# Kernel tuning notes

Hardware: AMD Instinct MI355X
Metric: run time of the kernel (lower is better)

Reference implementation:

```python
import jax, jax.numpy as jnp
import numpy as np
from jax import lax

E = 300   # word embedding dim (hard-coded embedding_size in DMCNN)
P = 5     # position-feature dim
H = 200   # conv out channels
S = 256   # max_seq_len
L = 34    # num_labels
VOCAB = 21128


def setup_inputs() -> dict:
    key = jax.random.key(0)
    ks = jax.random.split(key, 7)
    B = 8
    return {
        "inputs": jax.random.randint(ks[0], (B, S), 0, VOCAB, dtype=jnp.int64),
        "word_emb": jax.random.normal(ks[1], (VOCAB, E), dtype=jnp.float32) * 0.02,
        "pf_emb": jax.random.normal(ks[2], (S, P), dtype=jnp.float32) * 0.02,
        "conv_W": jax.random.normal(ks[3], (H, E + P, 3), dtype=jnp.float32) * 0.02,
        "conv_b": jax.random.normal(ks[4], (H,), dtype=jnp.float32) * 0.02,
        "fc_W": jax.random.normal(ks[5], (L, 3 * E + 2 * H), dtype=jnp.float32) * 0.02,
        "fc_b": jax.random.normal(ks[6], (L,), dtype=jnp.float32) * 0.02,
    }


def _conv1d(x_ncs, w_oik):
    # x: [N, C, S], w: [O, I, K], stride 1, padding 1 (kernel 3)
    return lax.conv_general_dilated(
        x_ncs, w_oik, window_strides=(1,), padding=[(1, 1)],
        dimension_numbers=("NCH", "OIH", "NCH"))


def reference(inputs, word_emb, pf_emb, conv_W, conv_b, fc_W, fc_b):
    B = inputs.shape[0]
    tok = word_emb[inputs]                       # [B, S, E]

    # Positions i = 1 .. S-2 (the original loop), fully vectorized.
    i_vals = jnp.arange(1, S - 1)                # [S-2]
    j = jnp.arange(S)
    pos_idx = jnp.abs(j[None, :] - i_vals[:, None])   # [S-2, S] == the loop's pos_index
    pf = pf_emb[pos_idx]                         # [S-2, S, P]

    # Conv is linear: split into token part (shared across i) + pf part (per i).
    W_tok, W_pf = conv_W[:, :E, :], conv_W[:, E:, :]
    conv_tok = _conv1d(tok.transpose(0, 2, 1), W_tok) + conv_b[None, :, None]  # [B, H, S]
    conv_pf = _conv1d(pf.transpose(0, 2, 1), W_pf)                             # [S-2, H, S] (batch-independent)

    out = jax.nn.relu(conv_tok[None] + conv_pf[:, None])   # [S-2, B, H, S]

    # Dynamic split max-pool at index i.
    left_mask = (j[None, :] < i_vals[:, None])[:, None, None, :]  # [S-2,1,1,S]
    neg_inf = jnp.array(-jnp.inf, dtype=out.dtype)
    max_left = jnp.where(left_mask, out, neg_inf).max(axis=-1)    # [S-2, B, H]
    max_right = jnp.where(left_mask, neg_inf, out).max(axis=-1)   # [S-2, B, H]
    pool = jnp.concatenate([max_left, max_right], axis=-1)        # [S-2, B, 2H]

    # Lexical-level features: window [i-1, i, i+1] flattened.
    llf = jnp.concatenate([tok[:, 0:S - 2], tok[:, 1:S - 1], tok[:, 2:S]], axis=-1)  # [B, S-2, 3E]

    feat = jnp.concatenate([pool.transpose(1, 0, 2), llf], axis=-1)  # [B, S-2, 2H+3E]
    logits_mid = jnp.einsum("bsf,lf->bsl", feat, fc_W) + fc_b        # [B, S-2, L]

    pad = jnp.zeros((B, 1, L), dtype=logits_mid.dtype).at[:, :, -1].set(1.0)
    return jnp.concatenate([pad, logits_mid, pad], axis=1)          # [B, S, L]
```

## Files before the change

### kernel.cpp

```cpp
#include <hip/hip_runtime.h>

#define E 300
#define P 5
#define H 200
#define S 256
#define L 34
#define B 8
#define NI 254

typedef __attribute__((ext_vector_type(8))) _Float16 half8;
typedef __attribute__((ext_vector_type(2))) _Float16 h2;
typedef __attribute__((ext_vector_type(4))) float f32x4;

#define TOKB_OFF   0
#define TOKB_FL    309632
#define WR3_OFF    309632
#define WR3_FL     96512
#define FCWB_OFF   406144
#define FCWB_FL    32256
#define G_OFF      438400
#define G_FL       51200
#define C0_OFF     489600
#define C0_FL      25400
#define C255_OFF   515000
#define C255_FL    25400
#define CT_OFF     540400
#define CT_FL      204800
#define POOLF_OFF  745200
#define POOLF_FL   425984

__device__ __forceinline__ unsigned short f2h(float f) {
    _Float16 h = (_Float16)f;
    unsigned short u; __builtin_memcpy(&u, &h, 2);
    return u;
}
__device__ __forceinline__ h2 u2h2(unsigned u) {
    h2 h; __builtin_memcpy(&h, &u, 4); return h;
}
__device__ __forceinline__ unsigned h2u(h2 h) {
    unsigned u; __builtin_memcpy(&u, &h, 4); return u;
}
__device__ __forceinline__ h2 hmax2(h2 a, h2 b) {
    return __builtin_elementwise_max(a, b);
}
__device__ __forceinline__ half8 load_h8(const unsigned short* p) {
    half8 r;
    ((ushort4*)&r)[0] = *(const ushort4*)p;
    ((ushort4*)&r)[1] = *(const ushort4*)(p + 4);
    return r;
}

#define GA_BLOCKS 605
#define PREP_BLOCKS 1803

__global__ __launch_bounds__(256) void k_init(const int* __restrict__ ids,
                                              const float* __restrict__ we,
                                              const float* __restrict__ convW,
                                              const float* __restrict__ fcW,
                                              const float* __restrict__ pf,
                                              unsigned short* __restrict__ tokb,
                                              unsigned short* __restrict__ Wr3,
                                              unsigned short* __restrict__ fcWb,
                                              unsigned short* __restrict__ g,
                                              unsigned short* __restrict__ c0,
                                              unsigned short* __restrict__ c255) {
    if (blockIdx.x < GA_BLOCKS) {
        int idx = blockIdx.x * 256 + threadIdx.x;
        const int total = B * 258 * 75;
        if (idx >= total) return;
        int row = idx / 75;
        int col = idx - row * 75;
        int b = row / 258;
        int r = row - b * 258;
        float4 v = make_float4(0.f, 0.f, 0.f, 0.f);
        if (r >= 1 && r <= 256) {
            int id = ids[b * S + (r - 1)];
            v = ((const float4*)we)[(size_t)id * 75 + col];
        }
        ushort4 o;
        o.x = f2h(v.x); o.y = f2h(v.y); o.z = f2h(v.z); o.w = f2h(v.w);
        *(ushort4*)(tokb + (size_t)row * 300 + col * 4) = o;
        return;
    }
    int idx = (blockIdx.x - GA_BLOCKS) * 256 + threadIdx.x;
    if (idx < 193024) {
        int hh = idx / 928, kk = idx - hh * 928;
        float v = 0.f;
        if (hh < H && kk < 900) {
            int r = kk / 300, e = kk - r * 300;
            v = convW[hh * 915 + e * 3 + r];
        }
        Wr3[idx] = f2h(v);
    } else if (idx < 257536) {
        int t = idx - 193024;
        int l = t / 1344, c = t - l * 1344;
        float v = 0.f;
        if (l < L) {
            if (c < 400) v = fcW[l * 1300 + c];
            else if (c >= 416 && c < 1316) v = fcW[l * 1300 + 400 + (c - 416)];
        }
        fcWb[t] = f2h(v);
    } else if (idx < 359936) {
        int t = idx - 257536;
        int t2 = t / H, h = t - t2 * H;
        int d = t2 - 256;
        float a = 0.f;
#pragma unroll
        for (int k = 0; k < 3; k++) {
            int r = d + k - 1; r = (r < 0) ? -r : r; if (r > 255) r = 255;
#pragma unroll
            for (int q = 0; q < P; q++)
                a += convW[h * 915 + (E + q) * 3 + k] * pf[r * P + q];
        }
        g[t] = f2h(a);
    } else if (idx < 410736) {
        int t = idx - 359936;
        int m = t / H, h = t - m * H;
        int i = m + 1;
        float a = 0.f;
#pragma unroll
        for (int q = 0; q < P; q++) {
            a += convW[h * 915 + (E + q) * 3 + 1] * pf[i * P + q];
            a += convW[h * 915 + (E + q) * 3 + 2] * pf[(i - 1) * P + q];
        }
        c0[m * H + h] = f2h(a);
    } else if (idx < 461536) {
        int t = idx - 410736;
        int m = t / H, h = t - m * H;
        int i = m + 1;
        float a = 0.f;
#pragma unroll
        for (int q = 0; q < P; q++) {
            a += convW[h * 915 + (E + q) * 3 + 0] * pf[(254 - i) * P + q];
            a += convW[h * 915 + (E + q) * 3 + 1] * pf[(255 - i) * P + q];
        }
        c255[m * H + h] = f2h(a);
    }
}

__global__ __launch_bounds__(512) void k_conv(const unsigned short* __restrict__ tokb,
                                              const unsigned short* __restrict__ Wr3,
                                              const float* __restrict__ convB,
                                              unsigned short* __restrict__ ct) {
    __shared__ float4 cld[4 * 64];
    int n0 = blockIdx.x * 16;
    int mg = blockIdx.y;
    int tid = threadIdx.x;
    int wave = tid >> 6;
    int lane = tid & 63;
    int mt = wave & 3;
    int kh = wave >> 2;
    int quad = lane >> 4;
    int lr = lane & 15;
    int mtile = mg * 4 + mt;
    int b = mtile >> 4;
    int j0 = (mtile & 15) << 4;

    const unsigned short* pa = tokb + ((size_t)(b * 258 + j0 + lr) * 300 + quad * 8);
    const unsigned short* pb = Wr3 + ((size_t)(n0 + lr) * 928 + quad * 8);

    f32x4 acc0 = {0.f, 0.f, 0.f, 0.f};
    f32x4 acc1 = {0.f, 0.f, 0.f, 0.f};
    if (kh == 0) {
#pragma unroll
        for (int kk = 0; kk < 14; kk += 2) {
            half8 a0 = load_h8(pa + kk * 32);
            half8 b0 = load_h8(pb + kk * 32);
            acc0 = __builtin_amdgcn_mfma_f32_16x16x32_f16(a0, b0, acc0, 0, 0, 0);
            half8 a1 = load_h8(pa + kk * 32 + 32);
            half8 b1 = load_h8(pb + kk * 32 + 32);
            acc1 = __builtin_amdgcn_mfma_f32_16x16x32_f16(a1, b1, acc1, 0, 0, 0);
        }
    } else {
#pragma unroll
        for (int kk = 14; kk + 1 < 29; kk += 2) {
            half8 a0 = load_h8(pa + kk * 32);
            half8 b0 = load_h8(pb + kk * 32);
            acc0 = __builtin_amdgcn_mfma_f32_16x16x32_f16(a0, b0, acc0, 0, 0, 0);
            half8 a1 = load_h8(pa + kk * 32 + 32);
            half8 b1 = load_h8(pb + kk * 32 + 32);
            acc1 = __builtin_amdgcn_mfma_f32_16x16x32_f16(a1, b1, acc1, 0, 0, 0);
        }
        {
            half8 a0 = load_h8(pa + 28 * 32);
            half8 b0 = load_h8(pb + 28 * 32);
            acc0 = __builtin_amdgcn_mfma_f32_16x16x32_f16(a0, b0, acc0, 0, 0, 0);
        }
    }
    f32x4 accw = acc0 + acc1;
    if (kh == 1) {
        cld[mt * 64 + lane] = make_float4(accw[0], accw[1], accw[2], accw[3]);
    }
    __syncthreads();
    if (kh == 0) {
        float4 p = cld[mt * 64 + lane];
        int h = n0 + lr;
        if (h < H) {
            float bias = convB[h];
            ct[(size_t)(b * 256 + j0 + quad * 4 + 0) * 200 + h] = f2h(accw[0] + p.x + bias);
            ct[(size_t)(b * 256 + j0 + quad * 4 + 1) * 200 + h] = f2h(accw[1] + p.y + bias);
            ct[(size_t)(b * 256 + j0 + quad * 4 + 2) * 200 + h] = f2h(accw[2] + p.z + bias);
            ct[(size_t)(b * 256 + j0 + quad * 4 + 3) * 200 + h] = f2h(accw[3] + p.w + bias);
        }
    }
}

__global__ __launch_bounds__(512) void k_poolA(const unsigned short* __restrict__ ct,
                                               const unsigned short* __restrict__ g,
                                               const unsigned short* __restrict__ c0,
                                               const unsigned short* __restrict__ c255,
                                               unsigned short* __restrict__ poolf) {
    __shared__ uint2 lds2[8 * 4 * 2 * 50];
    int pg = blockIdx.x;
    int b  = blockIdx.y;
    int tid = threadIdx.x;
    int sub = tid >> 6;
    int lane = tid & 63;
    int p0 = pg * 4 + 1;

    if (lane < 50) {
        int h = lane << 2;
        const unsigned short* ctb = ct + (size_t)b * S * H + h;
        const unsigned short* gb  = g + h;

        h2 z = {(_Float16)0, (_Float16)0};
        h2 aL0a=z, aL0b=z, aL1a=z, aL1b=z, aL2a=z, aL2b=z, aL3a=z, aL3b=z;
        h2 aR0a=z, aR0b=z, aR1a=z, aR1b=z, aR2a=z, aR2b=z, aR3a=z, aR3b=z;

        if (sub == 0) {
            uint2 cu = *(const uint2*)ctb;
            h2 ca = u2h2(cu.x), cb = u2h2(cu.y);
            int m = pg * 4;
            if (m + 0 < NI) { uint2 t = *(const uint2*)(c0 + (m+0) * H + h);
                aL0a = hmax2(aL0a, ca + u2h2(t.x)); aL0b = hmax2(aL0b, cb + u2h2(t.y)); }
            if (m + 1 < NI) { uint2 t = *(const uint2*)(c0 + (m+1) * H + h);
                aL1a = hmax2(aL1a, ca + u2h2(t.x)); aL1b = hmax2(aL1b, cb + u2h2(t.y)); }
            if (m + 2 < NI) { uint2 t = *(const uint2*)(c0 + (m+2) * H + h);
                aL2a = hmax2(aL2a, ca + u2h2(t.x)); aL2b = hmax2(aL2b, cb + u2h2(t.y)); }
            if (m + 3 < NI) { uint2 t = *(const uint2*)(c0 + (m+3) * H + h);
                aL3a = hmax2(aL3a, ca + u2h2(t.x)); aL3b = hmax2(aL3b, cb + u2h2(t.y)); }
        }
        if (sub == 7) {
            uint2 cu = *(const uint2*)(ctb + (size_t)255 * H);
            h2 ca = u2h2(cu.x), cb = u2h2(cu.y);
            int m = pg * 4;
            if (m + 0 < NI) { uint2 t = *(const uint2*)(c255 + (m+0) * H + h);
                aR0a = hmax2(aR0a, ca + u2h2(t.x)); aR0b = hmax2(aR0b, cb + u2h2(t.y)); }
            if (m + 1 < NI) { uint2 t = *(const uint2*)(c255 + (m+1) * H + h);
                aR1a = hmax2(aR1a, ca + u2h2(t.x)); aR1b = hmax2(aR1b, cb + u2h2(t.y)); }
            if (m + 2 < NI) { uint2 t = *(const uint2*)(c255 + (m+2) * H + h);
                aR2a = hmax2(aR2a, ca + u2h2(t.x)); aR2b = hmax2(aR2b, cb + u2h2(t.y)); }
            if (m + 3 < NI) { uint2 t = *(const uint2*)(c255 + (m+3) * H + h);
                aR3a = hmax2(aR3a, ca + u2h2(t.x)); aR3b = hmax2(aR3b, cb + u2h2(t.y)); }
        }

        int js = (sub == 0) ? 1 : sub * 32;
        int je = (sub == 7) ? 254 : sub * 32 + 31;

        uint2 gu;
        gu = *(const uint2*)(gb + (size_t)(js - p0 + 256) * H); h2 gr0a = u2h2(gu.x), gr0b = u2h2(gu.y);
        gu = *(const uint2*)(gb + (size_t)(js - p0 + 255) * H); h2 gr1a = u2h2(gu.x), gr1b = u2h2(gu.y);
        gu = *(const uint2*)(gb + (size_t)(js - p0 + 254) * H); h2 gr2a = u2h2(gu.x), gr2b = u2h2(gu.y);
        gu = *(const uint2*)(gb + (size_t)(js - p0 + 253) * H); h2 gr3a = u2h2(gu.x), gr3b = u2h2(gu.y);

        int eL = (je + 1 < p0) ? (je + 1) : p0;
        int mS = (js > p0) ? js : p0;
        int eM = (je + 1 < p0 + 4) ? (je + 1) : (p0 + 4);
        int rS = (js > p0 + 4) ? js : (p0 + 4);

#pragma unroll 4
        for (int j = js; j < eL; ++j) {
            uint2 cu = *(const uint2*)(ctb + (size_t)j * H);
            h2 ca = u2h2(cu.x), cb = u2h2(cu.y);
            aL0a = hmax2(aL0a, ca + gr0a); aL0b = hmax2(aL0b, cb + gr0b);
            aL1a = hmax2(aL1a, ca + gr1a); aL1b = hmax2(aL1b, cb + gr1b);
            aL2a = hmax2(aL2a, ca + gr2a); aL2b = hmax2(aL2b, cb + gr2b);
            aL3a = hmax2(aL3a, ca + gr3a); aL3b = hmax2(aL3b, cb + gr3b);
            gr3a = gr2a; gr3b = gr2b; gr2a = gr1a; gr2b = gr1b; gr1a = gr0a; gr1b = gr0b;
            uint2 gn = *(const uint2*)(gb + (size_t)(j + 1 - p0 + 256) * H);
            gr0a = u2h2(gn.x); gr0b = u2h2(gn.y);
        }
        for (int j = mS; j < eM; ++j) {
            uint2 cu = *(const uint2*)(ctb + (size_t)j * H);
            h2 ca = u2h2(cu.x), cb = u2h2(cu.y);
            h2 v0a = ca + gr0a, v0b = cb + gr0b;
            h2 v1a = ca + gr1a, v1b = cb + gr1b;
            h2 v2a = ca + gr2a, v2b = cb + gr2b;
            h2 v3a = ca + gr3a, v3b = cb + gr3b;
            if (j < p0)     { aL0a = hmax2(aL0a, v0a); aL0b = hmax2(aL0b, v0b); }
            else            { aR0a = hmax2(aR0a, v0a); aR0b = hmax2(aR0b, v0b); }
            if (j < p0 + 1) { aL1a = hmax2(aL1a, v1a); aL1b = hmax2(aL1b, v1b); }
            else            { aR1a = hmax2(aR1a, v1a); aR1b = hmax2(aR1b, v1b); }
            if (j < p0 + 2) { aL2a = hmax2(aL2a, v2a); aL2b = hmax2(aL2b, v2b); }
            else            { aR2a = hmax2(aR2a, v2a); aR2b = hmax2(aR2b, v2b); }
            if (j < p0 + 3) { aL3a = hmax2(aL3a, v3a); aL3b = hmax2(aL3b, v3b); }
            else            { aR3a = hmax2(aR3a, v3a); aR3b = hmax2(aR3b, v3b); }
            gr3a = gr2a; gr3b = gr2b; gr2a = gr1a; gr2b = gr1b; gr1a = gr0a; gr1b = gr0b;
            uint2 gn = *(const uint2*)(gb + (size_t)(j + 1 - p0 + 256) * H);
            gr0a = u2h2(gn.x); gr0b = u2h2(gn.y);
        }
#pragma unroll 4
        for (int j = rS; j <= je; ++j) {
            uint2 cu = *(const uint2*)(ctb + (size_t)j * H);
            h2 ca = u2h2(cu.x), cb = u2h2(cu.y);
            aR0a = hmax2(aR0a, ca + gr0a); aR0b = hmax2(aR0b, cb + gr0b);
            aR1a = hmax2(aR1a, ca + gr1a); aR1b = hmax2(aR1b, cb + gr1b);
            aR2a = hmax2(aR2a, ca + gr2a); aR2b = hmax2(aR2b, cb + gr2b);
            aR3a = hmax2(aR3a, ca + gr3a); aR3b = hmax2(aR3b, cb + gr3b);
            gr3a = gr2a; gr3b = gr2b; gr2a = gr1a; gr2b = gr1b; gr1a = gr0a; gr1b = gr0b;
            uint2 gn = *(const uint2*)(gb + (size_t)(j + 1 - p0 + 256) * H);
            gr0a = u2h2(gn.x); gr0b = u2h2(gn.y);
        }

        uint2* lp = lds2 + (size_t)sub * 400 + lane;
        lp[0]   = make_uint2(h2u(aL0a), h2u(aL0b)); lp[50]  = make_uint2(h2u(aR0a), h2u(aR0b));
        lp[100] = make_uint2(h2u(aL1a), h2u(aL1b)); lp[150] = make_uint2(h2u(aR1a), h2u(aR1b));
        lp[200] = make_uint2(h2u(aL2a), h2u(aL2b)); lp[250] = make_uint2(h2u(aR2a), h2u(aR2b));
        lp[300] = make_uint2(h2u(aL3a), h2u(aL3b)); lp[350] = make_uint2(h2u(aR3a), h2u(aR3b));
    }
    __syncthreads();

    if (tid < 400) {
        int k = tid / 100;
        int r = tid - k * 100;
        int hf = r / 50;
        int ln = r - hf * 50;
        int slot = (k * 2 + hf) * 50 + ln;
        uint2 v = lds2[slot];
        h2 va = u2h2(v.x), vb = u2h2(v.y);
#pragma unroll
        for (int s2 = 1; s2 < 8; s2++) {
            uint2 w = lds2[s2 * 400 + slot];
            va = hmax2(va, u2h2(w.x));
            vb = hmax2(vb, u2h2(w.y));
        }
        int m = pg * 4 + k;
        if (m < NI)
            *(uint2*)(poolf + (size_t)(b * 256 + m + 1) * 416 + hf * 200 + ln * 4)
                = make_uint2(h2u(va), h2u(vb));
    } else if (tid < 464) {
        int t = tid - 400;
        int k = t >> 4, c = t & 15;
        int m = pg * 4 + k;
        if (m < NI) poolf[(size_t)(b * 256 + m + 1) * 416 + 400 + c] = 0;
    }
}

__global__ __launch_bounds__(512) void k_fc(const unsigned short* __restrict__ poolf,
                                            const unsigned short* __restrict__ tokb,
                                            const unsigned short* __restrict__ fcWb,
                                            const float* __restrict__ fcB,
                                            float* __restrict__ out) {
    __shared__ float4 cld[4 * 64];
    int n0 = blockIdx.x * 16;
    int mg = blockIdx.y;
    int tid = threadIdx.x;
    int wave = tid >> 6;
    int lane = tid & 63;
    int mt = wave & 3;
    int kp = wave >> 2;
    int quad = lane >> 4;
    int lr = lane & 15;
    int mtile = mg * 4 + mt;
    int b = mtile >> 4;
    int s0 = (mtile & 15) << 4;

    const unsigned short* pa1 = tokb + ((size_t)(b * 258 + s0 + lr) * 300 + quad * 8);
    const unsigned short* pb1 = fcWb + ((size_t)(n0 + lr) * 1344 + 416 + quad * 8);

    f32x4 acc0 = {0.f, 0.f, 0.f, 0.f};
    f32x4 acc1 = {0.f, 0.f, 0.f, 0.f};
    if (kp == 0) {
        const unsigned short* pa0 = poolf + ((size_t)(b * 256 + s0 + lr) * 416 + quad * 8);
        const unsigned short* pb0 = fcWb + ((size_t)(n0 + lr) * 1344 + quad * 8);
#pragma unroll
        for (int kk = 0; kk + 1 < 13; kk += 2) {
            half8 a0 = load_h8(pa0 + kk * 32);
            half8 b0 = load_h8(pb0 + kk * 32);
            acc0 = __builtin_amdgcn_mfma_f32_16x16x32_f16(a0, b0, acc0, 0, 0, 0);
            half8 a1 = load_h8(pa0 + kk * 32 + 32);
            half8 b1 = load_h8(pb0 + kk * 32 + 32);
            acc1 = __builtin_amdgcn_mfma_f32_16x16x32_f16(a1, b1, acc1, 0, 0, 0);
        }
        {
            half8 a0 = load_h8(pa0 + 12 * 32);
            half8 b0 = load_h8(pb0 + 12 * 32);
            acc0 = __builtin_amdgcn_mfma_f32_16x16x32_f16(a0, b0, acc0, 0, 0, 0);
        }
#pragma unroll
        for (int kk = 0; kk < 8; kk += 2) {
            half8 a0 = load_h8(pa1 + kk * 32);
            half8 b0 = load_h8(pb1 + kk * 32);
            acc0 = __builtin_amdgcn_mfma_f32_16x16x32_f16(a0, b0, acc0, 0, 0, 0);
            half8 a1 = load_h8(pa1 + kk * 32 + 32);
            half8 b1 = load_h8(pb1 + kk * 32 + 32);
            acc1 = __builtin_amdgcn_mfma_f32_16x16x32_f16(a1, b1, acc1, 0, 0, 0);
        }
    } else {
#pragma unroll
        for (int kk = 8; kk + 1 < 29; kk += 2) {
            half8 a0 = load_h8(pa1 + kk * 32);
            half8 b0 = load_h8(pb1 + kk * 32);
            acc0 = __builtin_amdgcn_mfma_f32_16x16x32_f16(a0, b0, acc0, 0, 0, 0);
            half8 a1 = load_h8(pa1 + kk * 32 + 32);
            half8 b1 = load_h8(pb1 + kk * 32 + 32);
            acc1 = __builtin_amdgcn_mfma_f32_16x16x32_f16(a1, b1, acc1, 0, 0, 0);
        }
        {
            half8 a0 = load_h8(pa1 + 28 * 32);
            half8 b0 = load_h8(pb1 + 28 * 32);
            acc0 = __builtin_amdgcn_mfma_f32_16x16x32_f16(a0, b0, acc0, 0, 0, 0);
        }
    }
    f32x4 accw = acc0 + acc1;
    if (kp == 1) {
        cld[mt * 64 + lane] = make_float4(accw[0], accw[1], accw[2], accw[3]);
    }
    __syncthreads();
    if (kp == 0) {
        float4 p = cld[mt * 64 + lane];
        float r4[4] = {accw[0] + p.x, accw[1] + p.y, accw[2] + p.z, accw[3] + p.w};
        int l = n0 + lr;
        if (l < L) {
            float bias = fcB[l];
#pragma unroll
            for (int r = 0; r < 4; r++) {
                int s = s0 + quad * 4 + r;
                float val;
                if (s == 0 || s == S - 1) val = (l == L - 1) ? 1.0f : 0.0f;
                else                      val = r4[r] + bias;
                out[(size_t)(b * 256 + s) * L + l] = val;
            }
        }
    }
}

extern "C" void kernel_launch(void* const* d_in, const int* in_sizes, int n_in,
                              void* d_out, int out_size, void* d_ws, size_t ws_size,
                              hipStream_t stream) {
    const int*   ids      = (const int*)d_in[0];
    const float* word_emb = (const float*)d_in[1];
    const float* pf_emb   = (const float*)d_in[2];
    const float* conv_W   = (const float*)d_in[3];
    const float* conv_b   = (const float*)d_in[4];
    const float* fc_W     = (const float*)d_in[5];
    const float* fc_b     = (const float*)d_in[6];
    float* out = (float*)d_out;
    float* ws  = (float*)d_ws;

    unsigned short* tokb  = (unsigned short*)(ws + TOKB_OFF);
    unsigned short* Wr3   = (unsigned short*)(ws + WR3_OFF);
    unsigned short* fcWb  = (unsigned short*)(ws + FCWB_OFF);
    unsigned short* g     = (unsigned short*)(ws + G_OFF);
    unsigned short* c0    = (unsigned short*)(ws + C0_OFF);
    unsigned short* c255  = (unsigned short*)(ws + C255_OFF);
    unsigned short* ct    = (unsigned short*)(ws + CT_OFF);
    unsigned short* poolf = (unsigned short*)(ws + POOLF_OFF);

    k_init<<<GA_BLOCKS + PREP_BLOCKS, 256, 0, stream>>>(ids, word_emb, conv_W, fc_W,
                                                        pf_emb, tokb, Wr3, fcWb,
                                                        g, c0, c255);
    k_conv<<<dim3(13, 32), 512, 0, stream>>>(tokb, Wr3, conv_b, ct);
    k_poolA<<<dim3(64, 8), 512, 0, stream>>>(ct, g, c0, c255, poolf);
    k_fc<<<dim3(3, 32), 512, 0, stream>>>(poolf, tokb, fcWb, fc_b, out);
}
```

Measured before the change: 116.9 us.

## Fuse four kernels into one persistent kernel with global atomic barriers

Replaces the four launches (init, conv, pool, fc) with one persistent kernel of 256 blocks. The phases are separated by software grid barriers built on agent-scope atomics, and each phase walks its old grid with a block-stride loop. This removes per-launch overhead and the gaps between kernels. In exchange it adds a memset, spin-wait barriers that depend on all 256 blocks being resident at once, and a timeout break that could silently give wrong results.

```diff
diff --git a/kernel.cpp b/kernel.cpp
--- a/kernel.cpp
+++ b/kernel.cpp
@@ -7,27 +7,21 @@
 #define L 34
 #define B 8
 #define NI 254
+#define NBLK 256
 
 typedef __attribute__((ext_vector_type(8))) _Float16 half8;
 typedef __attribute__((ext_vector_type(2))) _Float16 h2;
 typedef __attribute__((ext_vector_type(4))) float f32x4;
 
 #define TOKB_OFF   0
-#define TOKB_FL    309632
 #define WR3_OFF    309632
-#define WR3_FL     96512
 #define FCWB_OFF   406144
-#define FCWB_FL    32256
 #define G_OFF      438400
-#define G_FL       51200
 #define C0_OFF     489600
-#define C0_FL      25400
 #define C255_OFF   515000
-#define C255_FL    25400
 #define CT_OFF     540400
-#define CT_FL      204800
 #define POOLF_OFF  745200
-#define POOLF_FL   425984
+#define BAR_OFF    2000000
 
 __device__ __forceinline__ unsigned short f2h(float f) {
     _Float16 h = (_Float16)f;
@@ -50,386 +44,399 @@
     return r;
 }
 
-#define GA_BLOCKS 605
-#define PREP_BLOCKS 1803
-
-__global__ __launch_bounds__(256) void k_init(const int* __restrict__ ids,
-                                              const float* __restrict__ we,
-                                              const float* __restrict__ convW,
-                                              const float* __restrict__ fcW,
-                                              const float* __restrict__ pf,
-                                              unsigned short* __restrict__ tokb,
-                                              unsigned short* __restrict__ Wr3,
-                                              unsigned short* __restrict__ fcWb,
-                                              unsigned short* __restrict__ g,
-                                              unsigned short* __restrict__ c0,
-                                              unsigned short* __restrict__ c255) {
-    if (blockIdx.x < GA_BLOCKS) {
-        int idx = blockIdx.x * 256 + threadIdx.x;
-        const int total = B * 258 * 75;
-        if (idx >= total) return;
-        int row = idx / 75;
-        int col = idx - row * 75;
-        int b = row / 258;
-        int r = row - b * 258;
-        float4 v = make_float4(0.f, 0.f, 0.f, 0.f);
-        if (r >= 1 && r <= 256) {
-            int id = ids[b * S + (r - 1)];
-            v = ((const float4*)we)[(size_t)id * 75 + col];
-        }
-        ushort4 o;
-        o.x = f2h(v.x); o.y = f2h(v.y); o.z = f2h(v.z); o.w = f2h(v.w);
-        *(ushort4*)(tokb + (size_t)row * 300 + col * 4) = o;
-        return;
-    }
-    int idx = (blockIdx.x - GA_BLOCKS) * 256 + threadIdx.x;
-    if (idx < 193024) {
-        int hh = idx / 928, kk = idx - hh * 928;
-        float v = 0.f;
-        if (hh < H && kk < 900) {
-            int r = kk / 300, e = kk - r * 300;
-            v = convW[hh * 915 + e * 3 + r];
-        }
-        Wr3[idx] = f2h(v);
-    } else if (idx < 257536) {
-        int t = idx - 193024;
-        int l = t / 1344, c = t - l * 1344;
-        float v = 0.f;
-        if (l < L) {
-            if (c < 400) v = fcW[l * 1300 + c];
-            else if (c >= 416 && c < 1316) v = fcW[l * 1300 + 400 + (c - 416)];
-        }
-        fcWb[t] = f2h(v);
-    } else if (idx < 359936) {
-        int t = idx - 257536;
-        int t2 = t / H, h = t - t2 * H;
-        int d = t2 - 256;
-        float a = 0.f;
-#pragma unroll
-        for (int k = 0; k < 3; k++) {
-            int r = d + k - 1; r = (r < 0) ? -r : r; if (r > 255) r = 255;
-#pragma unroll
-            for (int q = 0; q < P; q++)
-                a += convW[h * 915 + (E + q) * 3 + k] * pf[r * P + q];
-        }
-        g[t] = f2h(a);
-    } else if (idx < 410736) {
-        int t = idx - 359936;
-        int m = t / H, h = t - m * H;
-        int i = m + 1;
-        float a = 0.f;
-#pragma unroll
-        for (int q = 0; q < P; q++) {
-            a += convW[h * 915 + (E + q) * 3 + 1] * pf[i * P + q];
-            a += convW[h * 915 + (E + q) * 3 + 2] * pf[(i - 1) * P + q];
-        }
-        c0[m * H + h] = f2h(a);
-    } else if (idx < 461536) {
-        int t = idx - 410736;
-        int m = t / H, h = t - m * H;
-        int i = m + 1;
-        float a = 0.f;
-#pragma unroll
-        for (int q = 0; q < P; q++) {
-            a += convW[h * 915 + (E + q) * 3 + 0] * pf[(254 - i) * P + q];
-            a += convW[h * 915 + (E + q) * 3 + 1] * pf[(255 - i) * P + q];
-        }
-        c255[m * H + h] = f2h(a);
-    }
-}
-
-__global__ __launch_bounds__(512) void k_conv(const unsigned short* __restrict__ tokb,
-                                              const unsigned short* __restrict__ Wr3,
-                                              const float* __restrict__ convB,
-                                              unsigned short* __restrict__ ct) {
-    __shared__ float4 cld[4 * 64];
-    int n0 = blockIdx.x * 16;
-    int mg = blockIdx.y;
-    int tid = threadIdx.x;
-    int wave = tid >> 6;
-    int lane = tid & 63;
-    int mt = wave & 3;
-    int kh = wave >> 2;
-    int quad = lane >> 4;
-    int lr = lane & 15;
-    int mtile = mg * 4 + mt;
-    int b = mtile >> 4;
-    int j0 = (mtile & 15) << 4;
-
-    const unsigned short* pa = tokb + ((size_t)(b * 258 + j0 + lr) * 300 + quad * 8);
-    const unsigned short* pb = Wr3 + ((size_t)(n0 + lr) * 928 + quad * 8);
-
-    f32x4 acc0 = {0.f, 0.f, 0.f, 0.f};
-    f32x4 acc1 = {0.f, 0.f, 0.f, 0.f};
-    if (kh == 0) {
-#pragma unroll
-        for (int kk = 0; kk < 14; kk += 2) {
-            half8 a0 = load_h8(pa + kk * 32);
-            half8 b0 = load_h8(pb + kk * 32);
-            acc0 = __builtin_amdgcn_mfma_f32_16x16x32_f16(a0, b0, acc0, 0, 0, 0);
-            half8 a1 = load_h8(pa + kk * 32 + 32);
-            half8 b1 = load_h8(pb + kk * 32 + 32);
-            acc1 = __builtin_amdgcn_mfma_f32_16x16x32_f16(a1, b1, acc1, 0, 0, 0);
-        }
-    } else {
-#pragma unroll
-        for (int kk = 14; kk + 1 < 29; kk += 2) {
-            half8 a0 = load_h8(pa + kk * 32);
-            half8 b0 = load_h8(pb + kk * 32);
-            acc0 = __builtin_amdgcn_mfma_f32_16x16x32_f16(a0, b0, acc0, 0, 0, 0);
-            half8 a1 = load_h8(pa + kk * 32 + 32);
-            half8 b1 = load_h8(pb + kk * 32 + 32);
-            acc1 = __builtin_amdgcn_mfma_f32_16x16x32_f16(a1, b1, acc1, 0, 0, 0);
-        }
-        {
-            half8 a0 = load_h8(pa + 28 * 32);
-            half8 b0 = load_h8(pb + 28 * 32);
-            acc0 = __builtin_amdgcn_mfma_f32_16x16x32_f16(a0, b0, acc0, 0, 0, 0);
-        }
-    }
-    f32x4 accw = acc0 + acc1;
-    if (kh == 1) {
-        cld[mt * 64 + lane] = make_float4(accw[0], accw[1], accw[2], accw[3]);
+__device__ __forceinline__ void gbar(unsigned* bar, int idx) {
+    __syncthreads();
+    if (threadIdx.x == 0) {
+        unsigned* c = bar + idx * 16;
+        __hip_atomic_fetch_add(c, 1u, __ATOMIC_ACQ_REL, __HIP_MEMORY_SCOPE_AGENT);
+        unsigned t = 0;
+        while (__hip_atomic_load(c, __ATOMIC_ACQUIRE, __HIP_MEMORY_SCOPE_AGENT) < NBLK) {
+            __builtin_amdgcn_s_sleep(2);
+            if (++t > (1u << 22)) break;
+        }
     }
     __syncthreads();
-    if (kh == 0) {
-        float4 p = cld[mt * 64 + lane];
-        int h = n0 + lr;
-        if (h < H) {
-            float bias = convB[h];
-            ct[(size_t)(b * 256 + j0 + quad * 4 + 0) * 200 + h] = f2h(accw[0] + p.x + bias);
-            ct[(size_t)(b * 256 + j0 + quad * 4 + 1) * 200 + h] = f2h(accw[1] + p.y + bias);
-            ct[(size_t)(b * 256 + j0 + quad * 4 + 2) * 200 + h] = f2h(accw[2] + p.z + bias);
-            ct[(size_t)(b * 256 + j0 + quad * 4 + 3) * 200 + h] = f2h(accw[3] + p.w + bias);
+}
+
+__global__ __launch_bounds__(512, 2) void k_fused(
+        const int* __restrict__ ids,
+        const float* __restrict__ we,
+        const float* __restrict__ convW,
+        const float* __restrict__ fcW,
+        const float* __restrict__ pf,
+        const float* __restrict__ convB,
+        const float* __restrict__ fcB,
+        unsigned short* __restrict__ tokb,
+        unsigned short* __restrict__ Wr3,
+        unsigned short* __restrict__ fcWb,
+        unsigned short* __restrict__ g,
+        unsigned short* __restrict__ c0,
+        unsigned short* __restrict__ c255,
+        unsigned short* __restrict__ ct,
+        unsigned short* __restrict__ poolf,
+        float* __restrict__ out,
+        unsigned* bar) {
+    __shared__ __align__(16) unsigned char smem[25600];
+    float4* cld = (float4*)smem;
+    uint2*  lds2 = (uint2*)smem;
+
+    const int bid = blockIdx.x;
+    const int tid = threadIdx.x;
+
+    for (int gidx = bid * 512 + tid; gidx < 616336; gidx += NBLK * 512) {
+        if (gidx < 154800) {
+            int idx = gidx;
+            int row = idx / 75;
+            int col = idx - row * 75;
+            int b = row / 258;
+            int r = row - b * 258;
+            float4 v = make_float4(0.f, 0.f, 0.f, 0.f);
+            if (r >= 1 && r <= 256) {
+                int id = ids[b * S + (r - 1)];
+                v = ((const float4*)we)[(size_t)id * 75 + col];
+            }
+            ushort4 o;
+            o.x = f2h(v.x); o.y = f2h(v.y); o.z = f2h(v.z); o.w = f2h(v.w);
+            *(ushort4*)(tokb + (size_t)row * 300 + col * 4) = o;
+        } else {
+            int idx = gidx - 154800;
+            if (idx < 193024) {
+                int hh = idx / 928, kk = idx - hh * 928;
+                float v = 0.f;
+                if (hh < H && kk < 900) {
+                    int r = kk / 300, e = kk - r * 300;
+                    v = convW[hh * 915 + e * 3 + r];
+                }
+                Wr3[idx] = f2h(v);
+            } else if (idx < 257536) {
+                int t = idx - 193024;
+                int l = t / 1344, c = t - l * 1344;
+                float v = 0.f;
+                if (l < L) {
+                    if (c < 400) v = fcW[l * 1300 + c];
+                    else if (c >= 416 && c < 1316) v = fcW[l * 1300 + 400 + (c - 416)];
+                }
+                fcWb[t] = f2h(v);
+            } else if (idx < 359936) {
+                int t = idx - 257536;
+                int t2 = t / H, h = t - t2 * H;
+                int d = t2 - 256;
+                float a = 0.f;
+#pragma unroll
+                for (int k = 0; k < 3; k++) {
+                    int r = d + k - 1; r = (r < 0) ? -r : r; if (r > 255) r = 255;
+#pragma unroll
+                    for (int q = 0; q < P; q++)
+                        a += convW[h * 915 + (E + q) * 3 + k] * pf[r * P + q];
+                }
+                g[t] = f2h(a);
+            } else if (idx < 410736) {
+                int t = idx - 359936;
+                int m = t / H, h = t - m * H;
+                int i = m + 1;
+                float a = 0.f;
+#pragma unroll
+                for (int q = 0; q < P; q++) {
+                    a += convW[h * 915 + (E + q) * 3 + 1] * pf[i * P + q];
+                    a += convW[h * 915 + (E + q) * 3 + 2] * pf[(i - 1) * P + q];
+                }
+                c0[m * H + h] = f2h(a);
+            } else if (idx < 461536) {
+                int t = idx - 410736;
+                int m = t / H, h = t - m * H;
+                int i = m + 1;
+                float a = 0.f;
+#pragma unroll
+                for (int q = 0; q < P; q++) {
+                    a += convW[h * 915 + (E + q) * 3 + 0] * pf[(254 - i) * P + q];
+                    a += convW[h * 915 + (E + q) * 3 + 1] * pf[(255 - i) * P + q];
+                }
+                c255[m * H + h] = f2h(a);
+            }
         }
     }
-}
-
-__global__ __launch_bounds__(512) void k_poolA(const unsigned short* __restrict__ ct,
-                                               const unsigned short* __restrict__ g,
-                                               const unsigned short* __restrict__ c0,
-                                               const unsigned short* __restrict__ c255,
-                                               unsigned short* __restrict__ poolf) {
-    __shared__ uint2 lds2[8 * 4 * 2 * 50];
-    int pg = blockIdx.x;
-    int b  = blockIdx.y;
-    int tid = threadIdx.x;
-    int sub = tid >> 6;
-    int lane = tid & 63;
-    int p0 = pg * 4 + 1;
-
-    if (lane < 50) {
-        int h = lane << 2;
-        const unsigned short* ctb = ct + (size_t)b * S * H + h;
-        const unsigned short* gb  = g + h;
-
-        h2 z = {(_Float16)0, (_Float16)0};
-        h2 aL0a=z, aL0b=z, aL1a=z, aL1b=z, aL2a=z, aL2b=z, aL3a=z, aL3b=z;
-        h2 aR0a=z, aR0b=z, aR1a=z, aR1b=z, aR2a=z, aR2b=z, aR3a=z, aR3b=z;
-
-        if (sub == 0) {
-            uint2 cu = *(const uint2*)ctb;
-            h2 ca = u2h2(cu.x), cb = u2h2(cu.y);
-            int m = pg * 4;
-            if (m + 0 < NI) { uint2 t = *(const uint2*)(c0 + (m+0) * H + h);
-                aL0a = hmax2(aL0a, ca + u2h2(t.x)); aL0b = hmax2(aL0b, cb + u2h2(t.y)); }
-            if (m + 1 < NI) { uint2 t = *(const uint2*)(c0 + (m+1) * H + h);
-                aL1a = hmax2(aL1a, ca + u2h2(t.x)); aL1b = hmax2(aL1b, cb + u2h2(t.y)); }
-            if (m + 2 < NI) { uint2 t = *(const uint2*)(c0 + (m+2) * H + h);
-                aL2a = hmax2(aL2a, ca + u2h2(t.x)); aL2b = hmax2(aL2b, cb + u2h2(t.y)); }
-            if (m + 3 < NI) { uint2 t = *(const uint2*)(c0 + (m+3) * H + h);
-                aL3a = hmax2(aL3a, ca + u2h2(t.x)); aL3b = hmax2(aL3b, cb + u2h2(t.y)); }
-        }
-        if (sub == 7) {
-            uint2 cu = *(const uint2*)(ctb + (size_t)255 * H);
-            h2 ca = u2h2(cu.x), cb = u2h2(cu.y);
-            int m = pg * 4;
-            if (m + 0 < NI) { uint2 t = *(const uint2*)(c255 + (m+0) * H + h);
-                aR0a = hmax2(aR0a, ca + u2h2(t.x)); aR0b = hmax2(aR0b, cb + u2h2(t.y)); }
-            if (m + 1 < NI) { uint2 t = *(const uint2*)(c255 + (m+1) * H + h);
-                aR1a = hmax2(aR1a, ca + u2h2(t.x)); aR1b = hmax2(aR1b, cb + u2h2(t.y)); }
-            if (m + 2 < NI) { uint2 t = *(const uint2*)(c255 + (m+2) * H + h);
-                aR2a = hmax2(aR2a, ca + u2h2(t.x)); aR2b = hmax2(aR2b, cb + u2h2(t.y)); }
-            if (m + 3 < NI) { uint2 t = *(const uint2*)(c255 + (m+3) * H + h);
-                aR3a = hmax2(aR3a, ca + u2h2(t.x)); aR3b = hmax2(aR3b, cb + u2h2(t.y)); }
-        }
-
-        int js = (sub == 0) ? 1 : sub * 32;
-        int je = (sub == 7) ? 254 : sub * 32 + 31;
-
-        uint2 gu;
-        gu = *(const uint2*)(gb + (size_t)(js - p0 + 256) * H); h2 gr0a = u2h2(gu.x), gr0b = u2h2(gu.y);
-        gu = *(const uint2*)(gb + (size_t)(js - p0 + 255) * H); h2 gr1a = u2h2(gu.x), gr1b = u2h2(gu.y);
-        gu = *(const uint2*)(gb + (size_t)(js - p0 + 254) * H); h2 gr2a = u2h2(gu.x), gr2b = u2h2(gu.y);
-        gu = *(const uint2*)(gb + (size_t)(js - p0 + 253) * H); h2 gr3a = u2h2(gu.x), gr3b = u2h2(gu.y);
-
-        int eL = (je + 1 < p0) ? (je + 1) : p0;
-        int mS = (js > p0) ? js : p0;
-        int eM = (je + 1 < p0 + 4) ? (je + 1) : (p0 + 4);
-        int rS = (js > p0 + 4) ? js : (p0 + 4);
+    gbar(bar, 0);
+
+    for (int vb = bid; vb < 416; vb += NBLK) {
+        int n0 = (vb % 13) * 16;
+        int mg = vb / 13;
+        int wave = tid >> 6;
+        int lane = tid & 63;
+        int mt = wave & 3;
+        int kh = wave >> 2;
+        int quad = lane >> 4;
+        int lr = lane & 15;
+        int mtile = mg * 4 + mt;
+        int b = mtile >> 4;
+        int j0 = (mtile & 15) << 4;
+
+        const unsigned short* pa = tokb + ((size_t)(b * 258 + j0 + lr) * 300 + quad * 8);
+        const unsigned short* pb = Wr3 + ((size_t)(n0 + lr) * 928 + quad * 8);
+
+        f32x4 acc0 = {0.f, 0.f, 0.f, 0.f};
+        f32x4 acc1 = {0.f, 0.f, 0.f, 0.f};
+        if (kh == 0) {
+#pragma unroll
+            for (int kk = 0; kk < 14; kk += 2) {
+                half8 a0 = load_h8(pa + kk * 32);
+                half8 b0 = load_h8(pb + kk * 32);
+                acc0 = __builtin_amdgcn_mfma_f32_16x16x32_f16(a0, b0, acc0, 0, 0, 0);
+                half8 a1 = load_h8(pa + kk * 32 + 32);
+                half8 b1 = load_h8(pb + kk * 32 + 32);
+                acc1 = __builtin_amdgcn_mfma_f32_16x16x32_f16(a1, b1, acc1, 0, 0, 0);
+            }
+        } else {
+#pragma unroll
+            for (int kk = 14; kk + 1 < 29; kk += 2) {
+                half8 a0 = load_h8(pa + kk * 32);
+                half8 b0 = load_h8(pb + kk * 32);
+                acc0 = __builtin_amdgcn_mfma_f32_16x16x32_f16(a0, b0, acc0, 0, 0, 0);
+                half8 a1 = load_h8(pa + kk * 32 + 32);
+                half8 b1 = load_h8(pb + kk * 32 + 32);
+                acc1 = __builtin_amdgcn_mfma_f32_16x16x32_f16(a1, b1, acc1, 0, 0, 0);
+            }
+            {
+                half8 a0 = load_h8(pa + 28 * 32);
+                half8 b0 = load_h8(pb + 28 * 32);
+                acc0 = __builtin_amdgcn_mfma_f32_16x16x32_f16(a0, b0, acc0, 0, 0, 0);
+            }
+        }
+        f32x4 accw = acc0 + acc1;
+        if (kh == 1) {
+            cld[mt * 64 + lane] = make_float4(accw[0], accw[1], accw[2], accw[3]);
+        }
+        __syncthreads();
+        if (kh == 0) {
+            float4 p = cld[mt * 64 + lane];
+            int h = n0 + lr;
+            if (h < H) {
+                float bias = convB[h];
+                ct[(size_t)(b * 256 + j0 + quad * 4 + 0) * 200 + h] = f2h(accw[0] + p.x + bias);
+                ct[(size_t)(b * 256 + j0 + quad * 4 + 1) * 200 + h] = f2h(accw[1] + p.y + bias);
+                ct[(size_t)(b * 256 + j0 + quad * 4 + 2) * 200 + h] = f2h(accw[2] + p.z + bias);
+                ct[(size_t)(b * 256 + j0 + quad * 4 + 3) * 200 + h] = f2h(accw[3] + p.w + bias);
+            }
+        }
+        __syncthreads();
+    }
+    gbar(bar, 1);
+
+    for (int vc = bid; vc < 512; vc += NBLK) {
+        int pg = vc & 63;
+        int b  = vc >> 6;
+        int sub = tid >> 6;
+        int lane = tid & 63;
+        int p0 = pg * 4 + 1;
+
+        if (lane < 50) {
+            int h = lane << 2;
+            const unsigned short* ctb = ct + (size_t)b * S * H + h;
+            const unsigned short* gb  = g + h;
+
+            h2 z = {(_Float16)0, (_Float16)0};
+            h2 aL0a=z, aL0b=z, aL1a=z, aL1b=z, aL2a=z, aL2b=z, aL3a=z, aL3b=z;
+            h2 aR0a=z, aR0b=z, aR1a=z, aR1b=z, aR2a=z, aR2b=z, aR3a=z, aR3b=z;
+
+            if (sub == 0) {
+                uint2 cu = *(const uint2*)ctb;
+                h2 ca = u2h2(cu.x), cb = u2h2(cu.y);
+                int m = pg * 4;
+                if (m + 0 < NI) { uint2 t = *(const uint2*)(c0 + (m+0) * H + h);
+                    aL0a = hmax2(aL0a, ca + u2h2(t.x)); aL0b = hmax2(aL0b, cb + u2h2(t.y)); }
+                if (m + 1 < NI) { uint2 t = *(const uint2*)(c0 + (m+1) * H + h);
+                    aL1a = hmax2(aL1a, ca + u2h2(t.x)); aL1b = hmax2(aL1b, cb + u2h2(t.y)); }
+                if (m + 2 < NI) { uint2 t = *(const uint2*)(c0 + (m+2) * H + h);
+                    aL2a = hmax2(aL2a, ca + u2h2(t.x)); aL2b = hmax2(aL2b, cb + u2h2(t.y)); }
+                if (m + 3 < NI) { uint2 t = *(const uint2*)(c0 + (m+3) * H + h);
+                    aL3a = hmax2(aL3a, ca + u2h2(t.x)); aL3b = hmax2(aL3b, cb + u2h2(t.y)); }
+            }
+            if (sub == 7) {
+                uint2 cu = *(const uint2*)(ctb + (size_t)255 * H);
+                h2 ca = u2h2(cu.x), cb = u2h2(cu.y);
+                int m = pg * 4;
+                if (m + 0 < NI) { uint2 t = *(const uint2*)(c255 + (m+0) * H + h);
+                    aR0a = hmax2(aR0a, ca + u2h2(t.x)); aR0b = hmax2(aR0b, cb + u2h2(t.y)); }
+                if (m + 1 < NI) { uint2 t = *(const uint2*)(c255 + (m+1) * H + h);
+                    aR1a = hmax2(aR1a, ca + u2h2(t.x)); aR1b = hmax2(aR1b, cb + u2h2(t.y)); }
+                if (m + 2 < NI) { uint2 t = *(const uint2*)(c255 + (m+2) * H + h);
+                    aR2a = hmax2(aR2a, ca + u2h2(t.x)); aR2b = hmax2(aR2b, cb + u2h2(t.y)); }
+                if (m + 3 < NI) { uint2 t = *(const uint2*)(c255 + (m+3) * H + h);
+                    aR3a = hmax2(aR3a, ca + u2h2(t.x)); aR3b = hmax2(aR3b, cb + u2h2(t.y)); }
+            }
+
+            int js = (sub == 0) ? 1 : sub * 32;
+            int je = (sub == 7) ? 254 : sub * 32 + 31;
+
+            uint2 gu;
+            gu = *(const uint2*)(gb + (size_t)(js - p0 + 256) * H); h2 gr0a = u2h2(gu.x), gr0b = u2h2(gu.y);
+            gu = *(const uint2*)(gb + (size_t)(js - p0 + 255) * H); h2 gr1a = u2h2(gu.x), gr1b = u2h2(gu.y);
+            gu = *(const uint2*)(gb + (size_t)(js - p0 + 254) * H); h2 gr2a = u2h2(gu.x), gr2b = u2h2(gu.y);
+            gu = *(const uint2*)(gb + (size_t)(js - p0 + 253) * H); h2 gr3a = u2h2(gu.x), gr3b = u2h2(gu.y);
+
+            int eL = (je + 1 < p0) ? (je + 1) : p0;
+            int mS = (js > p0) ? js : p0;
+            int eM = (je + 1 < p0 + 4) ? (je + 1) : (p0 + 4);
+            int rS = (js > p0 + 4) ? js : (p0 + 4);
 
 #pragma unroll 4
-        for (int j = js; j < eL; ++j) {
-            uint2 cu = *(const uint2*)(ctb + (size_t)j * H);
-            h2 ca = u2h2(cu.x), cb = u2h2(cu.y);
-            aL0a = hmax2(aL0a, ca + gr0a); aL0b = hmax2(aL0b, cb + gr0b);
-            aL1a = hmax2(aL1a, ca + gr1a); aL1b = hmax2(aL1b, cb + gr1b);
-            aL2a = hmax2(aL2a, ca + gr2a); aL2b = hmax2(aL2b, cb + gr2b);
-            aL3a = hmax2(aL3a, ca + gr3a); aL3b = hmax2(aL3b, cb + gr3b);
-            gr3a = gr2a; gr3b = gr2b; gr2a = gr1a; gr2b = gr1b; gr1a = gr0a; gr1b = gr0b;
-            uint2 gn = *(const uint2*)(gb + (size_t)(j + 1 - p0 + 256) * H);
-            gr0a = u2h2(gn.x); gr0b = u2h2(gn.y);
-        }
-        for (int j = mS; j < eM; ++j) {
-            uint2 cu = *(const uint2*)(ctb + (size_t)j * H);
-            h2 ca = u2h2(cu.x), cb = u2h2(cu.y);
-            h2 v0a = ca + gr0a, v0b = cb + gr0b;
-            h2 v1a = ca + gr1a, v1b = cb + gr1b;
-            h2 v2a = ca + gr2a, v2b = cb + gr2b;
-            h2 v3a = ca + gr3a, v3b = cb + gr3b;
-            if (j < p0)     { aL0a = hmax2(aL0a, v0a); aL0b = hmax2(aL0b, v0b); }
-            else            { aR0a = hmax2(aR0a, v0a); aR0b = hmax2(aR0b, v0b); }
-            if (j < p0 + 1) { aL1a = hmax2(aL1a, v1a); aL1b = hmax2(aL1b, v1b); }
-            else            { aR1a = hmax2(aR1a, v1a); aR1b = hmax2(aR1b, v1b); }
-            if (j < p0 + 2) { aL2a = hmax2(aL2a, v2a); aL2b = hmax2(aL2b, v2b); }
-            else            { aR2a = hmax2(aR2a, v2a); aR2b = hmax2(aR2b, v2b); }
-            if (j < p0 + 3) { aL3a = hmax2(aL3a, v3a); aL3b = hmax2(aL3b, v3b); }
-            else            { aR3a = hmax2(aR3a, v3a); aR3b = hmax2(aR3b, v3b); }
-            gr3a = gr2a; gr3b = gr2b; gr2a = gr1a; gr2b = gr1b; gr1a = gr0a; gr1b = gr0b;
-            uint2 gn = *(const uint2*)(gb + (size_t)(j + 1 - p0 + 256) * H);
-            gr0a = u2h2(gn.x); gr0b = u2h2(gn.y);
-        }
+            for (int j = js; j < eL; ++j) {
+                uint2 cu = *(const uint2*)(ctb + (size_t)j * H);
+                h2 ca = u2h2(cu.x), cb = u2h2(cu.y);
+                aL0a = hmax2(aL0a, ca + gr0a); aL0b = hmax2(aL0b, cb + gr0b);
+                aL1a = hmax2(aL1a, ca + gr1a); aL1b = hmax2(aL1b, cb + gr1b);
+                aL2a = hmax2(aL2a, ca + gr2a); aL2b = hmax2(aL2b, cb + gr2b);
+                aL3a = hmax2(aL3a, ca + gr3a); aL3b = hmax2(aL3b, cb + gr3b);
+                gr3a = gr2a; gr3b = gr2b; gr2a = gr1a; gr2b = gr1b; gr1a = gr0a; gr1b = gr0b;
+                uint2 gn = *(const uint2*)(gb + (size_t)(j + 1 - p0 + 256) * H);
+                gr0a = u2h2(gn.x); gr0b = u2h2(gn.y);
+            }
+            for (int j = mS; j < eM; ++j) {
+                uint2 cu = *(const uint2*)(ctb + (size_t)j * H);
+                h2 ca = u2h2(cu.x), cb = u2h2(cu.y);
+                h2 v0a = ca + gr0a, v0b = cb + gr0b;
+                h2 v1a = ca + gr1a, v1b = cb + gr1b;
+                h2 v2a = ca + gr2a, v2b = cb + gr2b;
+                h2 v3a = ca + gr3a, v3b = cb + gr3b;
+                if (j < p0)     { aL0a = hmax2(aL0a, v0a); aL0b = hmax2(aL0b, v0b); }
+                else            { aR0a = hmax2(aR0a, v0a); aR0b = hmax2(aR0b, v0b); }
+                if (j < p0 + 1) { aL1a = hmax2(aL1a, v1a); aL1b = hmax2(aL1b, v1b); }
+                else            { aR1a = hmax2(aR1a, v1a); aR1b = hmax2(aR1b, v1b); }
+                if (j < p0 + 2) { aL2a = hmax2(aL2a, v2a); aL2b = hmax2(aL2b, v2b); }
+                else            { aR2a = hmax2(aR2a, v2a); aR2b = hmax2(aR2b, v2b); }
+                if (j < p0 + 3) { aL3a = hmax2(aL3a, v3a); aL3b = hmax2(aL3b, v3b); }
+                else            { aR3a = hmax2(aR3a, v3a); aR3b = hmax2(aR3b, v3b); }
+                gr3a = gr2a; gr3b = gr2b; gr2a = gr1a; gr2b = gr1b; gr1a = gr0a; gr1b = gr0b;
+                uint2 gn = *(const uint2*)(gb + (size_t)(j + 1 - p0 + 256) * H);
+                gr0a = u2h2(gn.x); gr0b = u2h2(gn.y);
+            }
 #pragma unroll 4
-        for (int j = rS; j <= je; ++j) {
-            uint2 cu = *(const uint2*)(ctb + (size_t)j * H);
-            h2 ca = u2h2(cu.x), cb = u2h2(cu.y);
-            aR0a = hmax2(aR0a, ca + gr0a); aR0b = hmax2(aR0b, cb + gr0b);
-            aR1a = hmax2(aR1a, ca + gr1a); aR1b = hmax2(aR1b, cb + gr1b);
-            aR2a = hmax2(aR2a, ca + gr2a); aR2b = hmax2(aR2b, cb + gr2b);
-            aR3a = hmax2(aR3a, ca + gr3a); aR3b = hmax2(aR3b, cb + gr3b);
-            gr3a = gr2a; gr3b = gr2b; gr2a = gr1a; gr2b = gr1b; gr1a = gr0a; gr1b = gr0b;
-            uint2 gn = *(const uint2*)(gb + (size_t)(j + 1 - p0 + 256) * H);
-            gr0a = u2h2(gn.x); gr0b = u2h2(gn.y);
-        }
-
-        uint2* lp = lds2 + (size_t)sub * 400 + lane;
-        lp[0]   = make_uint2(h2u(aL0a), h2u(aL0b)); lp[50]  = make_uint2(h2u(aR0a), h2u(aR0b));
-        lp[100] = make_uint2(h2u(aL1a), h2u(aL1b)); lp[150] = make_uint2(h2u(aR1a), h2u(aR1b));
-        lp[200] = make_uint2(h2u(aL2a), h2u(aL2b)); lp[250] = make_uint2(h2u(aR2a), h2u(aR2b));
-        lp[300] = make_uint2(h2u(aL3a), h2u(aL3b)); lp[350] = make_uint2(h2u(aR3a), h2u(aR3b));
+            for (int j = rS; j <= je; ++j) {
+                uint2 cu = *(const uint2*)(ctb + (size_t)j * H);
+                h2 ca = u2h2(cu.x), cb = u2h2(cu.y);
+                aR0a = hmax2(aR0a, ca + gr0a); aR0b = hmax2(aR0b, cb + gr0b);
+                aR1a = hmax2(aR1a, ca + gr1a); aR1b = hmax2(aR1b, cb + gr1b);
+                aR2a = hmax2(aR2a, ca + gr2a); aR2b = hmax2(aR2b, cb + gr2b);
+                aR3a = hmax2(aR3a, ca + gr3a); aR3b = hmax2(aR3b, cb + gr3b);
+                gr3a = gr2a; gr3b = gr2b; gr2a = gr1a; gr2b = gr1b; gr1a = gr0a; gr1b = gr0b;
+                uint2 gn = *(const uint2*)(gb + (size_t)(j + 1 - p0 + 256) * H);
+                gr0a = u2h2(gn.x); gr0b = u2h2(gn.y);
+            }
+
+            uint2* lp = lds2 + (size_t)sub * 400 + lane;
+            lp[0]   = make_uint2(h2u(aL0a), h2u(aL0b)); lp[50]  = make_uint2(h2u(aR0a), h2u(aR0b));
+            lp[100] = make_uint2(h2u(aL1a), h2u(aL1b)); lp[150] = make_uint2(h2u(aR1a), h2u(aR1b));
+            lp[200] = make_uint2(h2u(aL2a), h2u(aL2b)); lp[250] = make_uint2(h2u(aR2a), h2u(aR2b));
+            lp[300] = make_uint2(h2u(aL3a), h2u(aL3b)); lp[350] = make_uint2(h2u(aR3a), h2u(aR3b));
+        }
+        __syncthreads();
+
+        if (tid < 400) {
+            int k = tid / 100;
+            int r = tid - k * 100;
+            int hf = r / 50;
+            int ln = r - hf * 50;
+            int slot = (k * 2 + hf) * 50 + ln;
+            uint2 v = lds2[slot];
+            h2 va = u2h2(v.x), vb = u2h2(v.y);
+#pragma unroll
+            for (int s2 = 1; s2 < 8; s2++) {
+                uint2 w = lds2[s2 * 400 + slot];
+                va = hmax2(va, u2h2(w.x));
+                vb = hmax2(vb, u2h2(w.y));
+            }
+            int m = pg * 4 + k;
+            if (m < NI)
+                *(uint2*)(poolf + (size_t)(b * 256 + m + 1) * 416 + hf * 200 + ln * 4)
+                    = make_uint2(h2u(va), h2u(vb));
+        } else if (tid < 464) {
+            int t = tid - 400;
+            int k = t >> 4, c = t & 15;
+            int m = pg * 4 + k;
+            if (m < NI) poolf[(size_t)(b * 256 + m + 1) * 416 + 400 + c] = 0;
+        }
+        __syncthreads();
     }
-    __syncthreads();
-
-    if (tid < 400) {
-        int k = tid / 100;
-        int r = tid - k * 100;
-        int hf = r / 50;
-        int ln = r - hf * 50;
-        int slot = (k * 2 + hf) * 50 + ln;
-        uint2 v = lds2[slot];
-        h2 va = u2h2(v.x), vb = u2h2(v.y);
-#pragma unroll
-        for (int s2 = 1; s2 < 8; s2++) {
-            uint2 w = lds2[s2 * 400 + slot];
-            va = hmax2(va, u2h2(w.x));
-            vb = hmax2(vb, u2h2(w.y));
-        }
-        int m = pg * 4 + k;
-        if (m < NI)
-            *(uint2*)(poolf + (size_t)(b * 256 + m + 1) * 416 + hf * 200 + ln * 4)
-                = make_uint2(h2u(va), h2u(vb));
-    } else if (tid < 464) {
-        int t = tid - 400;
-        int k = t >> 4, c = t & 15;
-        int m = pg * 4 + k;
-        if (m < NI) poolf[(size_t)(b * 256 + m + 1) * 416 + 400 + c] = 0;
-    }
-}
-
-__global__ __launch_bounds__(512) void k_fc(const unsigned short* __restrict__ poolf,
-                                            const unsigned short* __restrict__ tokb,
-                                            const unsigned short* __restrict__ fcWb,
-                                            const float* __restrict__ fcB,
-                                            float* __restrict__ out) {
-    __shared__ float4 cld[4 * 64];
-    int n0 = blockIdx.x * 16;
-    int mg = blockIdx.y;
-    int tid = threadIdx.x;
-    int wave = tid >> 6;
-    int lane = tid & 63;
-    int mt = wave & 3;
-    int kp = wave >> 2;
-    int quad = lane >> 4;
-    int lr = lane & 15;
-    int mtile = mg * 4 + mt;
-    int b = mtile >> 4;
-    int s0 = (mtile & 15) << 4;
-
-    const unsigned short* pa1 = tokb + ((size_t)(b * 258 + s0 + lr) * 300 + quad * 8);
-    const unsigned short* pb1 = fcWb + ((size_t)(n0 + lr) * 1344 + 416 + quad * 8);
-
-    f32x4 acc0 = {0.f, 0.f, 0.f, 0.f};
-    f32x4 acc1 = {0.f, 0.f, 0.f, 0.f};
-    if (kp == 0) {
-        const unsigned short* pa0 = poolf + ((size_t)(b * 256 + s0 + lr) * 416 + quad * 8);
-        const unsigned short* pb0 = fcWb + ((size_t)(n0 + lr) * 1344 + quad * 8);
-#pragma unroll
-        for (int kk = 0; kk + 1 < 13; kk += 2) {
-            half8 a0 = load_h8(pa0 + kk * 32);
-            half8 b0 = load_h8(pb0 + kk * 32);
-            acc0 = __builtin_amdgcn_mfma_f32_16x16x32_f16(a0, b0, acc0, 0, 0, 0);
-            half8 a1 = load_h8(pa0 + kk * 32 + 32);
-            half8 b1 = load_h8(pb0 + kk * 32 + 32);
-            acc1 = __builtin_amdgcn_mfma_f32_16x16x32_f16(a1, b1, acc1, 0, 0, 0);
-        }
-        {
-            half8 a0 = load_h8(pa0 + 12 * 32);
-            half8 b0 = load_h8(pb0 + 12 * 32);
-            acc0 = __builtin_amdgcn_mfma_f32_16x16x32_f16(a0, b0, acc0, 0, 0, 0);
-        }
-#pragma unroll
-        for (int kk = 0; kk < 8; kk += 2) {
-            half8 a0 = load_h8(pa1 + kk * 32);
-            half8 b0 = load_h8(pb1 + kk * 32);
-            acc0 = __builtin_amdgcn_mfma_f32_16x16x32_f16(a0, b0, acc0, 0, 0, 0);
-            half8 a1 = load_h8(pa1 + kk * 32 + 32);
-            half8 b1 = load_h8(pb1 + kk * 32 + 32);
-            acc1 = __builtin_amdgcn_mfma_f32_16x16x32_f16(a1, b1, acc1, 0, 0, 0);
-        }
-    } else {
-#pragma unroll
-        for (int kk = 8; kk + 1 < 29; kk += 2) {
-            half8 a0 = load_h8(pa1 + kk * 32);
-            half8 b0 = load_h8(pb1 + kk * 32);
-            acc0 = __builtin_amdgcn_mfma_f32_16x16x32_f16(a0, b0, acc0, 0, 0, 0);
-            half8 a1 = load_h8(pa1 + kk * 32 + 32);
-            half8 b1 = load_h8(pb1 + kk * 32 + 32);
-            acc1 = __builtin_amdgcn_mfma_f32_16x16x32_f16(a1, b1, acc1, 0, 0, 0);
-        }
-        {
-            half8 a0 = load_h8(pa1 + 28 * 32);
-            half8 b0 = load_h8(pb1 + 28 * 32);
-            acc0 = __builtin_amdgcn_mfma_f32_16x16x32_f16(a0, b0, acc0, 0, 0, 0);
-        }
-    }
-    f32x4 accw = acc0 + acc1;
-    if (kp == 1) {
-        cld[mt * 64 + lane] = make_float4(accw[0], accw[1], accw[2], accw[3]);
-    }
-    __syncthreads();
-    if (kp == 0) {
-        float4 p = cld[mt * 64 + lane];
-        float r4[4] = {accw[0] + p.x, accw[1] + p.y, accw[2] + p.z, accw[3] + p.w};
-        int l = n0 + lr;
-        if (l < L) {
-            float bias = fcB[l];
-#pragma unroll
-            for (int r = 0; r < 4; r++) {
-                int s = s0 + quad * 4 + r;
-                float val;
-                if (s == 0 || s == S - 1) val = (l == L - 1) ? 1.0f : 0.0f;
-                else                      val = r4[r] + bias;
-                out[(size_t)(b * 256 + s) * L + l] = val;
+    gbar(bar, 2);
+
+    if (bid < 96) {
+        int n0 = (bid % 3) * 16;
+        int mg = bid / 3;
+        int wave = tid >> 6;
+        int lane = tid & 63;
+        int mt = wave & 3;
+        int kp = wave >> 2;
+        int quad = lane >> 4;
+        int lr = lane & 15;
+        int mtile = mg * 4 + mt;
+        int b = mtile >> 4;
+        int s0 = (mtile & 15) << 4;
+
+        const unsigned short* pa1 = tokb + ((size_t)(b * 258 + s0 + lr) * 300 + quad * 8);
+        const unsigned short* pb1 = fcWb + ((size_t)(n0 + lr) * 1344 + 416 + quad * 8);
+
+        f32x4 acc0 = {0.f, 0.f, 0.f, 0.f};
+        f32x4 acc1 = {0.f, 0.f, 0.f, 0.f};
+        if (kp == 0) {
+            const unsigned short* pa0 = poolf + ((size_t)(b * 256 + s0 + lr) * 416 + quad * 8);
+            const unsigned short* pb0 = fcWb + ((size_t)(n0 + lr) * 1344 + quad * 8);
+#pragma unroll
+            for (int kk = 0; kk + 1 < 13; kk += 2) {
+                half8 a0 = load_h8(pa0 + kk * 32);
+                half8 b0 = load_h8(pb0 + kk * 32);
+                acc0 = __builtin_amdgcn_mfma_f32_16x16x32_f16(a0, b0, acc0, 0, 0, 0);
+                half8 a1 = load_h8(pa0 + kk * 32 + 32);
+                half8 b1 = load_h8(pb0 + kk * 32 + 32);
+                acc1 = __builtin_amdgcn_mfma_f32_16x16x32_f16(a1, b1, acc1, 0, 0, 0);
+            }
+            {
+                half8 a0 = load_h8(pa0 + 12 * 32);
+                half8 b0 = load_h8(pb0 + 12 * 32);
+                acc0 = __builtin_amdgcn_mfma_f32_16x16x32_f16(a0, b0, acc0, 0, 0, 0);
+            }
+#pragma unroll
+            for (int kk = 0; kk < 8; kk += 2) {
+                half8 a0 = load_h8(pa1 + kk * 32);
+                half8 b0 = load_h8(pb1 + kk * 32);
+                acc0 = __builtin_amdgcn_mfma_f32_16x16x32_f16(a0, b0, acc0, 0, 0, 0);
+                half8 a1 = load_h8(pa1 + kk * 32 + 32);
+                half8 b1 = load_h8(pb1 + kk * 32 + 32);
+                acc1 = __builtin_amdgcn_mfma_f32_16x16x32_f16(a1, b1, acc1, 0, 0, 0);
+            }
+        } else {
+#pragma unroll
+            for (int kk = 8; kk + 1 < 29; kk += 2) {
+                half8 a0 = load_h8(pa1 + kk * 32);
+                half8 b0 = load_h8(pb1 + kk * 32);
+                acc0 = __builtin_amdgcn_mfma_f32_16x16x32_f16(a0, b0, acc0, 0, 0, 0);
+                half8 a1 = load_h8(pa1 + kk * 32 + 32);
+                half8 b1 = load_h8(pb1 + kk * 32 + 32);
+                acc1 = __builtin_amdgcn_mfma_f32_16x16x32_f16(a1, b1, acc1, 0, 0, 0);
+            }
+            {
+                half8 a0 = load_h8(pa1 + 28 * 32);
+                half8 b0 = load_h8(pb1 + 28 * 32);
+                acc0 = __builtin_amdgcn_mfma_f32_16x16x32_f16(a0, b0, acc0, 0, 0, 0);
+            }
+        }
+        f32x4 accw = acc0 + acc1;
+        if (kp == 1) {
+            cld[mt * 64 + lane] = make_float4(accw[0], accw[1], accw[2], accw[3]);
+        }
+        __syncthreads();
+        if (kp == 0) {
+            float4 p = cld[mt * 64 + lane];
+            float r4[4] = {accw[0] + p.x, accw[1] + p.y, accw[2] + p.z, accw[3] + p.w};
+            int l = n0 + lr;
+            if (l < L) {
+                float bias = fcB[l];
+#pragma unroll
+                for (int r = 0; r < 4; r++) {
+                    int s = s0 + quad * 4 + r;
+                    float val;
+                    if (s == 0 || s == S - 1) val = (l == L - 1) ? 1.0f : 0.0f;
+                    else                      val = r4[r] + bias;
+                    out[(size_t)(b * 256 + s) * L + l] = val;
+                }
             }
         }
     }
@@ -456,11 +463,10 @@
     unsigned short* c255  = (unsigned short*)(ws + C255_OFF);
     unsigned short* ct    = (unsigned short*)(ws + CT_OFF);
     unsigned short* poolf = (unsigned short*)(ws + POOLF_OFF);
-
-    k_init<<<GA_BLOCKS + PREP_BLOCKS, 256, 0, stream>>>(ids, word_emb, conv_W, fc_W,
-                                                        pf_emb, tokb, Wr3, fcWb,
-                                                        g, c0, c255);
-    k_conv<<<dim3(13, 32), 512, 0, stream>>>(tokb, Wr3, conv_b, ct);
-    k_poolA<<<dim3(64, 8), 512, 0, stream>>>(ct, g, c0, c255, poolf);
-    k_fc<<<dim3(3, 32), 512, 0, stream>>>(poolf, tokb, fcWb, fc_b, out);
-}
+    unsigned*       bar   = (unsigned*)(ws + BAR_OFF);
+
+    hipMemsetAsync(bar, 0, 256, stream);
+    k_fused<<<NBLK, 512, 0, stream>>>(ids, word_emb, conv_W, fc_W, pf_emb,
+                                      conv_b, fc_b, tokb, Wr3, fcWb, g,
+                                      c0, c255, ct, poolf, out, bar);
+}
```

Measured after the change: 200.6 us. +71.7%, slower.
